# Performance work log

Hardware: AMD Instinct MI355X
Metric: run time of the kernel (lower is better)

The kernel has to match this reference:

```python
import jax, jax.numpy as jnp
import numpy as np

SEQ_LEN, BATCH, INPUT_DIM, HIDDEN_DIM = 2048, 16, 1024, 2048
COMPRESSION_RATIO = 0.5


def setup_inputs() -> dict:
    key = jax.random.key(0)
    ks = jax.random.split(key, 10)
    s_in = 0.02  # xavier-ish scale for (hidden, input) linears
    return {
        "x": jax.random.normal(ks[0], (SEQ_LEN, BATCH, INPUT_DIM), dtype=jnp.float32),
        "A": jax.random.normal(ks[1], (HIDDEN_DIM, HIDDEN_DIM), dtype=jnp.float32) * 0.1 - 0.5,
        "W_B": jax.random.normal(ks[2], (HIDDEN_DIM, INPUT_DIM), dtype=jnp.float32) * s_in,
        "W_C": jax.random.normal(ks[3], (HIDDEN_DIM, INPUT_DIM), dtype=jnp.float32) * s_in,
        "W_delta": jax.random.normal(ks[4], (HIDDEN_DIM, INPUT_DIM), dtype=jnp.float32) * s_in,
        "b_delta": jnp.zeros((HIDDEN_DIM,), dtype=jnp.float32),
        "W_in": jax.random.normal(ks[5], (HIDDEN_DIM, INPUT_DIM), dtype=jnp.float32) * s_in,
        "b_in": jnp.zeros((HIDDEN_DIM,), dtype=jnp.float32),
        "W_comp": jax.random.normal(ks[6], (INPUT_DIM, HIDDEN_DIM), dtype=jnp.float32) * s_in,
        "b_comp": jnp.zeros((INPUT_DIM,), dtype=jnp.float32),
    }


def reference(x, A, W_B, W_C, W_delta, b_delta, W_in, b_in, W_comp, b_comp):
    # x: (S, B, D_in).  A is an unused parameter in the original forward.
    seq_len = x.shape[0]
    compressed_len = max(1, int(seq_len * COMPRESSION_RATIO))
    step = seq_len // compressed_len

    # Batched projections over all timesteps (replaces per-step Linears)
    B_all = jnp.einsum('sbd,hd->sbh', x, W_B)                       # (S, B, H)
    C_all = jnp.einsum('sbd,hd->sbh', x, W_C)                       # (S, B, H)
    delta = jax.nn.softplus(jnp.einsum('sbd,hd->sbh', x, W_delta) + b_delta)
    u = jnp.einsum('sbd,hd->sbh', x, W_in) + b_in + B_all           # x_proj + B_t

    # Gated linear recurrence: h_t = (1 - delta_t) * h_{t-1} + delta_t * u_t
    def step_fn(h, inp):
        d, uu = inp
        h = (1.0 - d) * h + d * uu
        return h, h

    h0 = jnp.zeros((x.shape[1], u.shape[-1]), dtype=x.dtype)
    _, hs = jax.lax.scan(step_fn, h0, (delta, u))                   # (S, B, H)

    y = C_all * hs                                                  # (S, B, H)

    # Output at the last timestep of each window of size `step`
    idx = np.array([min(i + step, seq_len) - 1 for i in range(0, seq_len, step)])
    y_sel = y[idx]                                                  # (S_c, B, H)
    return jnp.einsum('sbh,dh->sbd', y_sel, W_comp) + b_comp        # (S_c, B, D_in)
```

## Files before the change

kernel.cpp:

```cpp
#include <hip/hip_runtime.h>
#include <hip/hip_bf16.h>
#include <cstdio>

#define S_LEN 2048
#define BATCH 16
#define D_INP 1024
#define H_DIM 2048
#define SC    (S_LEN / 2)
#define BH    (BATCH * H_DIM)
#define NC    16
#define CS    (S_LEN / NC)

typedef __bf16 b16;
typedef __bf16 b16x8 __attribute__((ext_vector_type(8)));
typedef __bf16 b16x4 __attribute__((ext_vector_type(4)));
typedef float  f32x4 __attribute__((ext_vector_type(4)));

__device__ __forceinline__ int sw_off(int r, int k8) {
  return r * 32 + ((k8 ^ ((r >> 1) & 3)) << 3);
}

__device__ __forceinline__ void gl2lds16(const b16* g, b16* l) {
  __builtin_amdgcn_global_load_lds(
      (const __attribute__((address_space(1))) void*)g,
      (__attribute__((address_space(3))) void*)l, 16, 0, 0);
}

__device__ __forceinline__ float softplus_fast(float t) {
  float e = __expf(-fabsf(t));
  return fmaxf(t, 0.f) + __logf(1.f + e);
}

__global__ void cvt_x_kernel(const float* __restrict__ in, b16* __restrict__ out, int n4) {
  int i = blockIdx.x * 256 + threadIdx.x;
  if (i >= n4) return;
  float4 v = ((const float4*)in)[i];
  b16x4 o = {(b16)v.x, (b16)v.y, (b16)v.z, (b16)v.w};
  ((b16x4*)out)[i] = o;
}

__global__ void prep_w_kernel(const float* __restrict__ Wd, const float* __restrict__ Win,
                              const float* __restrict__ WB, const float* __restrict__ Wc,
                              const float* __restrict__ Wcp,
                              b16* __restrict__ Wdu, b16* __restrict__ Wcb,
                              b16* __restrict__ Wcpb) {
  const int HD4 = (H_DIM * D_INP) / 4;
  int i = blockIdx.x * 256 + threadIdx.x;
  if (i >= HD4) return;
  float4 a = ((const float4*)Wd)[i];
  float4 b = ((const float4*)Win)[i];
  float4 c = ((const float4*)WB)[i];
  float4 d = ((const float4*)Wc)[i];
  float4 e = ((const float4*)Wcp)[i];
  ((b16x4*)Wdu)[i] = {(b16)a.x, (b16)a.y, (b16)a.z, (b16)a.w};
  ((b16x4*)Wdu)[HD4 + i] = {(b16)(b.x + c.x), (b16)(b.y + c.y), (b16)(b.z + c.z), (b16)(b.w + c.w)};
  ((b16x4*)Wcb)[i] = {(b16)d.x, (b16)d.y, (b16)d.z, (b16)d.w};
  ((b16x4*)Wcpb)[i] = {(b16)e.x, (b16)e.y, (b16)e.z, (b16)e.w};
}

#define AH0 0
#define AH1 8192
#define BH0 16384
#define BH1 24576

template <int MODE>
__device__ __forceinline__ void stage_half(const b16* __restrict__ G, int ldg,
                                           int base_row, int kcol, b16* half_base,
                                           int wave, int lane, bool isA) {
#pragma unroll
  for (int q = 0; q < 2; ++q) {
    const int rbase = q * 128 + wave * 16;
    const int r = rbase + (lane >> 2);
    const int p = lane & 3;
    const int gl = p ^ ((r >> 1) & 3);
    long grow = base_row + r;
    if (MODE == 1 && isA) grow = 2 * grow - (grow & 15) + 16;
    gl2lds16(G + grow * (long)ldg + kcol + gl * 8, half_base + rbase * 32);
  }
}

template <int MODE>
__global__ __launch_bounds__(512, 2) void gemm8p(
    const b16* __restrict__ A, const b16* __restrict__ W, int K,
    const float* __restrict__ bias0, const float* __restrict__ bias1,
    const b16* __restrict__ hsel, b16* __restrict__ ob0, b16* __restrict__ ob1,
    float* __restrict__ of) {
  extern __shared__ b16 lds[];
  const int tid  = threadIdx.x;
  const int lane = tid & 63;
  const int wave = tid >> 6;
  const int wm = wave >> 2, wn = wave & 3;
  const int lm = lane & 15;
  const int l8 = lane >> 4;

  const int gx  = gridDim.x;
  const int nwg = gx * gridDim.y;
  const int id0 = blockIdx.y * gx + blockIdx.x;
  const int sw  = (id0 & 7) * (nwg >> 3) + (id0 >> 3);
  const int m0 = (sw / gx) * 256;
  const int n0 = (sw % gx) * 256;

  f32x4 acc[8][4];
#pragma unroll
  for (int i = 0; i < 8; i++)
#pragma unroll
    for (int j = 0; j < 4; j++) acc[i][j] = (f32x4)0.f;

  const int NT = K >> 6;

  {
    b16* B0 = lds;
    stage_half<MODE>(A, K, m0, 0,  B0 + AH0, wave, lane, true);
    stage_half<MODE>(W, K, n0, 0,  B0 + BH0, wave, lane, false);
    stage_half<MODE>(A, K, m0, 32, B0 + AH1, wave, lane, true);
    stage_half<MODE>(W, K, n0, 32, B0 + BH1, wave, lane, false);
    asm volatile("s_waitcnt vmcnt(4)" ::: "memory");
    __builtin_amdgcn_s_barrier();
  }

  for (int t = 0; t < NT; ++t) {
    b16* const C = lds + ((t & 1) << 15);
    b16* const N = lds + (((t + 1) & 1) << 15);
    const int kn = (t + 1) << 6;
    const bool pf = (t + 1 < NT);
    b16x8 a[8], bb0, bb1;

#pragma unroll
    for (int i = 0; i < 8; i++)
      a[i] = *(const b16x8*)(C + AH0 + sw_off(wm * 128 + i * 16 + lm, l8));
    bb0 = *(const b16x8*)(C + BH0 + sw_off(wn * 64 + 0 + lm, l8));
    bb1 = *(const b16x8*)(C + BH0 + sw_off(wn * 64 + 16 + lm, l8));
    if (pf) stage_half<MODE>(A, K, m0, kn, N + AH0, wave, lane, true);
    __builtin_amdgcn_s_barrier();
    asm volatile("s_waitcnt lgkmcnt(0)" ::: "memory");
    __builtin_amdgcn_sched_barrier(0);
    __builtin_amdgcn_s_setprio(1);
#pragma unroll
    for (int i = 0; i < 8; i++) {
      acc[i][0] = __builtin_amdgcn_mfma_f32_16x16x32_bf16(a[i], bb0, acc[i][0], 0, 0, 0);
      acc[i][1] = __builtin_amdgcn_mfma_f32_16x16x32_bf16(a[i], bb1, acc[i][1], 0, 0, 0);
    }
    __builtin_amdgcn_s_setprio(0);
    __builtin_amdgcn_s_barrier();

    bb0 = *(const b16x8*)(C + BH0 + sw_off(wn * 64 + 32 + lm, l8));
    bb1 = *(const b16x8*)(C + BH0 + sw_off(wn * 64 + 48 + lm, l8));
    if (pf) {
      stage_half<MODE>(W, K, n0, kn, N + BH0, wave, lane, false);
      asm volatile("s_waitcnt vmcnt(4)" ::: "memory");
    } else {
      asm volatile("s_waitcnt vmcnt(0)" ::: "memory");
    }
    __builtin_amdgcn_s_barrier();
    asm volatile("s_waitcnt lgkmcnt(0)" ::: "memory");
    __builtin_amdgcn_sched_barrier(0);
    __builtin_amdgcn_s_setprio(1);
#pragma unroll
    for (int i = 0; i < 8; i++) {
      acc[i][2] = __builtin_amdgcn_mfma_f32_16x16x32_bf16(a[i], bb0, acc[i][2], 0, 0, 0);
      acc[i][3] = __builtin_amdgcn_mfma_f32_16x16x32_bf16(a[i], bb1, acc[i][3], 0, 0, 0);
    }
    __builtin_amdgcn_s_setprio(0);
    __builtin_amdgcn_s_barrier();

#pragma unroll
    for (int i = 0; i < 8; i++)
      a[i] = *(const b16x8*)(C + AH1 + sw_off(wm * 128 + i * 16 + lm, l8));
    bb0 = *(const b16x8*)(C + BH1 + sw_off(wn * 64 + 0 + lm, l8));
    bb1 = *(const b16x8*)(C + BH1 + sw_off(wn * 64 + 16 + lm, l8));
    if (pf) stage_half<MODE>(A, K, m0, kn + 32, N + AH1, wave, lane, true);
    __builtin_amdgcn_s_barrier();
    asm volatile("s_waitcnt lgkmcnt(0)" ::: "memory");
    __builtin_amdgcn_sched_barrier(0);
    __builtin_amdgcn_s_setprio(1);
#pragma unroll
    for (int i = 0; i < 8; i++) {
      acc[i][0] = __builtin_amdgcn_mfma_f32_16x16x32_bf16(a[i], bb0, acc[i][0], 0, 0, 0);
      acc[i][1] = __builtin_amdgcn_mfma_f32_16x16x32_bf16(a[i], bb1, acc[i][1], 0, 0, 0);
    }
    __builtin_amdgcn_s_setprio(0);
    __builtin_amdgcn_s_barrier();

    bb0 = *(const b16x8*)(C + BH1 + sw_off(wn * 64 + 32 + lm, l8));
    bb1 = *(const b16x8*)(C + BH1 + sw_off(wn * 64 + 48 + lm, l8));
    if (pf) {
      stage_half<MODE>(W, K, n0, kn + 32, N + BH1, wave, lane, false);
      asm volatile("s_waitcnt vmcnt(4)" ::: "memory");
    }
    __builtin_amdgcn_s_barrier();
    asm volatile("s_waitcnt lgkmcnt(0)" ::: "memory");
    __builtin_amdgcn_sched_barrier(0);
    __builtin_amdgcn_s_setprio(1);
#pragma unroll
    for (int i = 0; i < 8; i++) {
      acc[i][2] = __builtin_amdgcn_mfma_f32_16x16x32_bf16(a[i], bb0, acc[i][2], 0, 0, 0);
      acc[i][3] = __builtin_amdgcn_mfma_f32_16x16x32_bf16(a[i], bb1, acc[i][3], 0, 0, 0);
    }
    __builtin_amdgcn_s_setprio(0);
    __builtin_amdgcn_s_barrier();
  }

  if (MODE == 0) {
    const bool is_delta = (n0 < H_DIM);
    const float* bias = is_delta ? bias0 : bias1;
    b16* ob = is_delta ? ob0 : ob1;
    const int nc0 = (n0 & (H_DIM - 1)) + wn * 64 + lm;
    float bv[4];
#pragma unroll
    for (int j = 0; j < 4; j++) bv[j] = bias[nc0 + j * 16];
#pragma unroll
    for (int i = 0; i < 8; i++) {
      const long rb = m0 + wm * 128 + i * 16 + l8 * 4;
      b16* pr = ob + rb * H_DIM + nc0;
      if (is_delta) {
#pragma unroll
        for (int j = 0; j < 4; j++)
#pragma unroll
          for (int rg = 0; rg < 4; ++rg)
            pr[(long)rg * H_DIM + j * 16] = (b16)softplus_fast(acc[i][j][rg] + bv[j]);
      } else {
#pragma unroll
        for (int j = 0; j < 4; j++)
#pragma unroll
          for (int rg = 0; rg < 4; ++rg)
            pr[(long)rg * H_DIM + j * 16] = (b16)(acc[i][j][rg] + bv[j]);
      }
    }
  } else if (MODE == 1) {
    const int nc0 = n0 + wn * 64 + lm;
#pragma unroll
    for (int i = 0; i < 8; i++) {
      const long rb = m0 + wm * 128 + i * 16 + l8 * 4;
      const b16* hp = hsel + rb * H_DIM + nc0;
      b16* pr = ob0 + rb * H_DIM + nc0;
#pragma unroll
      for (int j = 0; j < 4; j++)
#pragma unroll
        for (int rg = 0; rg < 4; ++rg) {
          float hv = (float)hp[(long)rg * H_DIM + j * 16];
          pr[(long)rg * H_DIM + j * 16] = (b16)(acc[i][j][rg] * hv);
        }
    }
  } else {
    const int nc0 = n0 + wn * 64 + lm;
    float bv[4];
#pragma unroll
    for (int j = 0; j < 4; j++) bv[j] = bias0[nc0 + j * 16];
#pragma unroll
    for (int i = 0; i < 8; i++) {
      const long rb = m0 + wm * 128 + i * 16 + l8 * 4;
      float* pr = of + rb * D_INP + nc0;
#pragma unroll
      for (int j = 0; j < 4; j++)
#pragma unroll
        for (int rg = 0; rg < 4; ++rg)
          pr[(long)rg * D_INP + j * 16] = acc[i][j][rg] + bv[j];
    }
  }
}

__device__ __forceinline__ int sw_off128(int r, int k8) {
  return r * 32 + ((k8 ^ ((r >> 1) & 3)) << 3);
}

template <int MODE>
__global__ __launch_bounds__(256, 2) void gemm_bt(
    const b16* __restrict__ A, const b16* __restrict__ W, int K,
    const float* __restrict__ bias0, const float* __restrict__ bias1,
    const b16* __restrict__ hsel, b16* __restrict__ ob0, b16* __restrict__ ob1,
    float* __restrict__ of) {
  __shared__ b16 As[128 * 32];
  __shared__ b16 Bs[128 * 32];
  const int tid  = threadIdx.x;
  const int lane = tid & 63;
  const int wave = tid >> 6;
  const int wr = wave >> 1, wc = wave & 1;
  const int m0 = blockIdx.y * 128;
  const int n0 = blockIdx.x * 128;
  const int lm = lane & 15;
  const int l8 = lane >> 4;
  const int rL  = wave * 16 + (lane >> 2);
  const int k8p = lane & 3;

  f32x4 acc[4][4];
#pragma unroll
  for (int i = 0; i < 4; i++)
#pragma unroll
    for (int j = 0; j < 4; j++) acc[i][j] = (f32x4)0.f;

  for (int k0 = 0; k0 < K; k0 += 32) {
#pragma unroll
    for (int hh = 0; hh < 2; ++hh) {
      const int r = rL + hh * 64;
      const int k8l = k8p ^ ((r >> 1) & 3);
      b16* ldsA = As + (wave * 16 + hh * 64) * 32;
      b16* ldsB = Bs + (wave * 16 + hh * 64) * 32;
      long arow = m0 + r;
      if (MODE == 1) arow = 2 * arow - (arow & 15) + 16;
      gl2lds16(A + arow * (long)K + k0 + k8l * 8, ldsA);
      gl2lds16(W + (long)(n0 + r) * K + k0 + k8l * 8, ldsB);
    }
    __syncthreads();
    b16x8 af[4], bfr[4];
#pragma unroll
    for (int i = 0; i < 4; i++) af[i] = *(const b16x8*)(As + sw_off128(wr * 64 + i * 16 + lm, l8));
#pragma unroll
    for (int j = 0; j < 4; j++) bfr[j] = *(const b16x8*)(Bs + sw_off128(wc * 64 + j * 16 + lm, l8));
#pragma unroll
    for (int i = 0; i < 4; i++)
#pragma unroll
      for (int j = 0; j < 4; j++)
        acc[i][j] = __builtin_amdgcn_mfma_f32_16x16x32_bf16(af[i], bfr[j], acc[i][j], 0, 0, 0);
    __syncthreads();
  }

  if (MODE == 0) {
    const bool is_delta = (n0 < H_DIM);
    const float* bias = is_delta ? bias0 : bias1;
    b16* ob = is_delta ? ob0 : ob1;
    const int nc0 = (n0 & (H_DIM - 1)) + wc * 64 + lm;
    float bv[4];
#pragma unroll
    for (int j = 0; j < 4; j++) bv[j] = bias[nc0 + j * 16];
#pragma unroll
    for (int i = 0; i < 4; i++) {
      const long rb = m0 + wr * 64 + i * 16 + l8 * 4;
      b16* pr = ob + rb * H_DIM + nc0;
      if (is_delta) {
#pragma unroll
        for (int j = 0; j < 4; j++)
#pragma unroll
          for (int rg = 0; rg < 4; ++rg)
            pr[(long)rg * H_DIM + j * 16] = (b16)softplus_fast(acc[i][j][rg] + bv[j]);
      } else {
#pragma unroll
        for (int j = 0; j < 4; j++)
#pragma unroll
          for (int rg = 0; rg < 4; ++rg)
            pr[(long)rg * H_DIM + j * 16] = (b16)(acc[i][j][rg] + bv[j]);
      }
    }
  } else if (MODE == 1) {
    const int nc0 = n0 + wc * 64 + lm;
#pragma unroll
    for (int i = 0; i < 4; i++) {
      const long rb = m0 + wr * 64 + i * 16 + l8 * 4;
      const b16* hp = hsel + rb * H_DIM + nc0;
      b16* pr = ob0 + rb * H_DIM + nc0;
#pragma unroll
      for (int j = 0; j < 4; j++)
#pragma unroll
        for (int rg = 0; rg < 4; ++rg) {
          float hv = (float)hp[(long)rg * H_DIM + j * 16];
          pr[(long)rg * H_DIM + j * 16] = (b16)(acc[i][j][rg] * hv);
        }
    }
  } else {
    const int nc0 = n0 + wc * 64 + lm;
    float bv[4];
#pragma unroll
    for (int j = 0; j < 4; j++) bv[j] = bias0[nc0 + j * 16];
#pragma unroll
    for (int i = 0; i < 4; i++) {
      const long rb = m0 + wr * 64 + i * 16 + l8 * 4;
      float* pr = of + rb * D_INP + nc0;
#pragma unroll
      for (int j = 0; j < 4; j++)
#pragma unroll
        for (int rg = 0; rg < 4; ++rg)
          pr[(long)rg * D_INP + j * 16] = acc[i][j][rg] + bv[j];
    }
  }
}

__global__ void scan_a_kernel(const b16* __restrict__ dl, const b16* __restrict__ uu,
                              float* __restrict__ P, float* __restrict__ Q) {
  int g = blockIdx.x * 256 + threadIdx.x;
  int c = g >> 15;
  int p = g & (BH - 1);
  const b16* dp = dl + (size_t)c * CS * BH + p;
  const b16* up = uu + (size_t)c * CS * BH + p;
  float h = 0.f, pr = 1.f;
#pragma unroll 4
  for (int s = 0; s < CS; ++s) {
    float d = (float)dp[(size_t)s * BH];
    float u = (float)up[(size_t)s * BH];
    float a = 1.f - d;
    h = a * h + d * u;
    pr *= a;
  }
  P[g] = pr;
  Q[g] = h;
}

__global__ void scan_b_kernel(const float* __restrict__ P, const float* __restrict__ Q,
                              float* __restrict__ Hs) {
  int p = blockIdx.x * 256 + threadIdx.x;
  float h = 0.f;
#pragma unroll
  for (int c = 0; c < NC; ++c) {
    Hs[c * BH + p] = h;
    h = P[c * BH + p] * h + Q[c * BH + p];
  }
}

__global__ void scan_c_kernel(const b16* __restrict__ dl, const b16* __restrict__ uu,
                              const float* __restrict__ Hs, b16* __restrict__ hsel) {
  int g = blockIdx.x * 256 + threadIdx.x;
  int c = g >> 15;
  int p = g & (BH - 1);
  const b16* dp = dl + (size_t)c * CS * BH + p;
  const b16* up = uu + (size_t)c * CS * BH + p;
  b16* hp = hsel + (size_t)(c * (CS / 2)) * BH + p;
  float h = Hs[g];
#pragma unroll 4
  for (int s = 0; s < CS; ++s) {
    float d = (float)dp[(size_t)s * BH];
    float u = (float)up[(size_t)s * BH];
    h = (1.f - d) * h + d * u;
    if (s & 1) hp[(size_t)(s >> 1) * BH] = (b16)h;
  }
}

extern "C" void kernel_launch(void* const* d_in, const int* in_sizes, int n_in,
                              void* d_out, int out_size, void* d_ws, size_t ws_size,
                              hipStream_t stream) {
  const float* x   = (const float*)d_in[0];
  const float* WB  = (const float*)d_in[2];
  const float* Wc  = (const float*)d_in[3];
  const float* Wd  = (const float*)d_in[4];
  const float* bd  = (const float*)d_in[5];
  const float* Win = (const float*)d_in[6];
  const float* bi  = (const float*)d_in[7];
  const float* Wcp = (const float*)d_in[8];
  const float* bc  = (const float*)d_in[9];
  float* out = (float*)d_out;

  char* w = (char*)d_ws;
  size_t off = 0;
  auto alloc = [&](size_t bytes) {
    void* p = w + off;
    off += (bytes + 255) & ~(size_t)255;
    return p;
  };
  b16* xb   = (b16*)alloc((size_t)S_LEN * BATCH * D_INP * 2);
  b16* Wdu  = (b16*)alloc((size_t)2 * H_DIM * D_INP * 2);
  b16* Wcb  = (b16*)alloc((size_t)H_DIM * D_INP * 2);
  b16* Wcpb = (b16*)alloc((size_t)D_INP * H_DIM * 2);
  b16* dbuf = (b16*)alloc((size_t)S_LEN * BH * 2);
  b16* ubuf = (b16*)alloc((size_t)S_LEN * BH * 2);
  b16* hsel = (b16*)alloc((size_t)SC * BH * 2);
  b16* ysel = (b16*)alloc((size_t)SC * BH * 2);
  float* P  = (float*)alloc((size_t)NC * BH * 4);
  float* Q  = (float*)alloc((size_t)NC * BH * 4);
  float* Hs = (float*)alloc((size_t)NC * BH * 4);
  if (off > ws_size) {
    fprintf(stderr, "kernel_launch: ws too small: need %zu have %zu\n", off, ws_size);
    return;
  }

  static int g_big = -1;
  if (g_big < 0) {
    hipError_t e0 = hipFuncSetAttribute(reinterpret_cast<const void*>(&gemm8p<0>),
                                        hipFuncAttributeMaxDynamicSharedMemorySize, 131072);
    hipError_t e1 = hipFuncSetAttribute(reinterpret_cast<const void*>(&gemm8p<1>),
                                        hipFuncAttributeMaxDynamicSharedMemorySize, 131072);
    hipError_t e2 = hipFuncSetAttribute(reinterpret_cast<const void*>(&gemm8p<2>),
                                        hipFuncAttributeMaxDynamicSharedMemorySize, 131072);
    g_big = (e0 == hipSuccess && e1 == hipSuccess && e2 == hipSuccess) ? 1 : 0;
  }

  int n4 = S_LEN * BATCH * D_INP / 4;
  cvt_x_kernel<<<(n4 + 255) / 256, 256, 0, stream>>>(x, xb, n4);
  int hd4 = H_DIM * D_INP / 4;
  prep_w_kernel<<<(hd4 + 255) / 256, 256, 0, stream>>>(Wd, Win, WB, Wc, Wcp, Wdu, Wcb, Wcpb);
  if (g_big) {
    dim3 g1(2 * H_DIM / 256, S_LEN * BATCH / 256);
    gemm8p<0><<<g1, 512, 131072, stream>>>(xb, Wdu, D_INP, bd, bi, nullptr, dbuf, ubuf, nullptr);
  } else {
    dim3 g1(2 * H_DIM / 128, S_LEN * BATCH / 128);
    gemm_bt<0><<<g1, 256, 0, stream>>>(xb, Wdu, D_INP, bd, bi, nullptr, dbuf, ubuf, nullptr);
  }
  scan_a_kernel<<<NC * BH / 256, 256, 0, stream>>>(dbuf, ubuf, P, Q);
  scan_b_kernel<<<BH / 256, 256, 0, stream>>>(P, Q, Hs);
  scan_c_kernel<<<NC * BH / 256, 256, 0, stream>>>(dbuf, ubuf, Hs, hsel);
  if (g_big) {
    dim3 g2(H_DIM / 256, SC * BATCH / 256);
    gemm8p<1><<<g2, 512, 131072, stream>>>(xb, Wcb, D_INP, nullptr, nullptr, hsel, ysel, nullptr, nullptr);
  } else {
    dim3 g2(H_DIM / 128, SC * BATCH / 128);
    gemm_bt<1><<<g2, 256, 0, stream>>>(xb, Wcb, D_INP, nullptr, nullptr, hsel, ysel, nullptr, nullptr);
  }
  if (g_big) {
    dim3 g3(D_INP / 256, SC * BATCH / 256);
    gemm8p<2><<<g3, 512, 131072, stream>>>(ysel, Wcpb, H_DIM, bc, nullptr, nullptr, nullptr, nullptr, out);
  } else {
    dim3 g3(D_INP / 128, SC * BATCH / 128);
    gemm_bt<2><<<g3, 256, 0, stream>>>(ysel, Wcpb, H_DIM, bc, nullptr, nullptr, nullptr, nullptr, out);
  }
}
```

Measured before the change: 811.7 us.

## Reorder GEMM main loop into 4x4 MFMA quadrants and vectorize scan kernels

```diff
diff --git a/kernel.cpp b/kernel.cpp
--- a/kernel.cpp
+++ b/kernel.cpp
@@ -8,6 +8,7 @@
 #define H_DIM 2048
 #define SC    (S_LEN / 2)
 #define BH    (BATCH * H_DIM)
+#define BH8   (BH / 8)
 #define NC    16
 #define CS    (S_LEN / NC)
 
@@ -31,12 +32,14 @@
   return fmaxf(t, 0.f) + __logf(1.f + e);
 }
 
-__global__ void cvt_x_kernel(const float* __restrict__ in, b16* __restrict__ out, int n4) {
+__global__ void cvt_x_kernel(const float* __restrict__ in, b16* __restrict__ out, int n8) {
   int i = blockIdx.x * 256 + threadIdx.x;
-  if (i >= n4) return;
-  float4 v = ((const float4*)in)[i];
-  b16x4 o = {(b16)v.x, (b16)v.y, (b16)v.z, (b16)v.w};
-  ((b16x4*)out)[i] = o;
+  if (i >= n8) return;
+  float4 v0 = ((const float4*)in)[i * 2];
+  float4 v1 = ((const float4*)in)[i * 2 + 1];
+  b16x8 o = {(b16)v0.x, (b16)v0.y, (b16)v0.z, (b16)v0.w,
+             (b16)v1.x, (b16)v1.y, (b16)v1.z, (b16)v1.w};
+  ((b16x8*)out)[i] = o;
 }
 
 __global__ void prep_w_kernel(const float* __restrict__ Wd, const float* __restrict__ Win,
@@ -79,6 +82,18 @@
   }
 }
 
+#define MFMA16(AF, BF, ROW0)                                                       \
+  do {                                                                             \
+    __builtin_amdgcn_s_setprio(1);                                                 \
+    _Pragma("unroll") for (int i_ = 0; i_ < 4; i_++) {                             \
+      _Pragma("unroll") for (int j_ = 0; j_ < 4; j_++) {                           \
+        acc[ROW0 + i_][j_] = __builtin_amdgcn_mfma_f32_16x16x32_bf16(              \
+            AF[i_], BF[j_], acc[ROW0 + i_][j_], 0, 0, 0);                          \
+      }                                                                            \
+    }                                                                              \
+    __builtin_amdgcn_s_setprio(0);                                                 \
+  } while (0)
+
 template <int MODE>
 __global__ __launch_bounds__(512, 2) void gemm8p(
     const b16* __restrict__ A, const b16* __restrict__ W, int K,
@@ -108,14 +123,21 @@
 
   const int NT = K >> 6;
 
+  b16x8 aE[4], aO[4], b0f[4], b1f[4];
+
   {
-    b16* B0 = lds;
-    stage_half<MODE>(A, K, m0, 0,  B0 + AH0, wave, lane, true);
-    stage_half<MODE>(W, K, n0, 0,  B0 + BH0, wave, lane, false);
-    stage_half<MODE>(A, K, m0, 32, B0 + AH1, wave, lane, true);
-    stage_half<MODE>(W, K, n0, 32, B0 + BH1, wave, lane, false);
+    stage_half<MODE>(A, K, m0, 0,  lds + AH0, wave, lane, true);
+    stage_half<MODE>(W, K, n0, 0,  lds + BH0, wave, lane, false);
+    stage_half<MODE>(A, K, m0, 32, lds + AH1, wave, lane, true);
+    stage_half<MODE>(W, K, n0, 32, lds + BH1, wave, lane, false);
     asm volatile("s_waitcnt vmcnt(4)" ::: "memory");
     __builtin_amdgcn_s_barrier();
+#pragma unroll
+    for (int i = 0; i < 4; i++)
+      aE[i] = *(const b16x8*)(lds + AH0 + sw_off(wm * 128 + i * 16 + lm, l8));
+#pragma unroll
+    for (int j = 0; j < 4; j++)
+      b0f[j] = *(const b16x8*)(lds + BH0 + sw_off(wn * 64 + j * 16 + lm, l8));
   }
 
   for (int t = 0; t < NT; ++t) {
@@ -123,28 +145,17 @@
     b16* const N = lds + (((t + 1) & 1) << 15);
     const int kn = (t + 1) << 6;
     const bool pf = (t + 1 < NT);
-    b16x8 a[8], bb0, bb1;
-
-#pragma unroll
-    for (int i = 0; i < 8; i++)
-      a[i] = *(const b16x8*)(C + AH0 + sw_off(wm * 128 + i * 16 + lm, l8));
-    bb0 = *(const b16x8*)(C + BH0 + sw_off(wn * 64 + 0 + lm, l8));
-    bb1 = *(const b16x8*)(C + BH0 + sw_off(wn * 64 + 16 + lm, l8));
+
     if (pf) stage_half<MODE>(A, K, m0, kn, N + AH0, wave, lane, true);
     __builtin_amdgcn_s_barrier();
-    asm volatile("s_waitcnt lgkmcnt(0)" ::: "memory");
+#pragma unroll
+    for (int i = 0; i < 4; i++)
+      aO[i] = *(const b16x8*)(C + AH0 + sw_off(wm * 128 + 64 + i * 16 + lm, l8));
+    asm volatile("s_waitcnt lgkmcnt(4)" ::: "memory");
     __builtin_amdgcn_sched_barrier(0);
-    __builtin_amdgcn_s_setprio(1);
-#pragma unroll
-    for (int i = 0; i < 8; i++) {
-      acc[i][0] = __builtin_amdgcn_mfma_f32_16x16x32_bf16(a[i], bb0, acc[i][0], 0, 0, 0);
-      acc[i][1] = __builtin_amdgcn_mfma_f32_16x16x32_bf16(a[i], bb1, acc[i][1], 0, 0, 0);
-    }
-    __builtin_amdgcn_s_setprio(0);
-    __builtin_amdgcn_s_barrier();
-
-    bb0 = *(const b16x8*)(C + BH0 + sw_off(wn * 64 + 32 + lm, l8));
-    bb1 = *(const b16x8*)(C + BH0 + sw_off(wn * 64 + 48 + lm, l8));
+    MFMA16(aE, b0f, 0);
+    __builtin_amdgcn_s_barrier();
+
     if (pf) {
       stage_half<MODE>(W, K, n0, kn, N + BH0, wave, lane, false);
       asm volatile("s_waitcnt vmcnt(4)" ::: "memory");
@@ -152,51 +163,45 @@
       asm volatile("s_waitcnt vmcnt(0)" ::: "memory");
     }
     __builtin_amdgcn_s_barrier();
-    asm volatile("s_waitcnt lgkmcnt(0)" ::: "memory");
+#pragma unroll
+    for (int i = 0; i < 4; i++)
+      aE[i] = *(const b16x8*)(C + AH1 + sw_off(wm * 128 + i * 16 + lm, l8));
+#pragma unroll
+    for (int j = 0; j < 4; j++)
+      b1f[j] = *(const b16x8*)(C + BH1 + sw_off(wn * 64 + j * 16 + lm, l8));
+    asm volatile("s_waitcnt lgkmcnt(8)" ::: "memory");
     __builtin_amdgcn_sched_barrier(0);
-    __builtin_amdgcn_s_setprio(1);
-#pragma unroll
-    for (int i = 0; i < 8; i++) {
-      acc[i][2] = __builtin_amdgcn_mfma_f32_16x16x32_bf16(a[i], bb0, acc[i][2], 0, 0, 0);
-      acc[i][3] = __builtin_amdgcn_mfma_f32_16x16x32_bf16(a[i], bb1, acc[i][3], 0, 0, 0);
-    }
-    __builtin_amdgcn_s_setprio(0);
-    __builtin_amdgcn_s_barrier();
-
-#pragma unroll
-    for (int i = 0; i < 8; i++)
-      a[i] = *(const b16x8*)(C + AH1 + sw_off(wm * 128 + i * 16 + lm, l8));
-    bb0 = *(const b16x8*)(C + BH1 + sw_off(wn * 64 + 0 + lm, l8));
-    bb1 = *(const b16x8*)(C + BH1 + sw_off(wn * 64 + 16 + lm, l8));
+    MFMA16(aO, b0f, 4);
+    __builtin_amdgcn_s_barrier();
+
     if (pf) stage_half<MODE>(A, K, m0, kn + 32, N + AH1, wave, lane, true);
     __builtin_amdgcn_s_barrier();
-    asm volatile("s_waitcnt lgkmcnt(0)" ::: "memory");
+#pragma unroll
+    for (int i = 0; i < 4; i++)
+      aO[i] = *(const b16x8*)(C + AH1 + sw_off(wm * 128 + 64 + i * 16 + lm, l8));
+    asm volatile("s_waitcnt lgkmcnt(4)" ::: "memory");
     __builtin_amdgcn_sched_barrier(0);
-    __builtin_amdgcn_s_setprio(1);
-#pragma unroll
-    for (int i = 0; i < 8; i++) {
-      acc[i][0] = __builtin_amdgcn_mfma_f32_16x16x32_bf16(a[i], bb0, acc[i][0], 0, 0, 0);
-      acc[i][1] = __builtin_amdgcn_mfma_f32_16x16x32_bf16(a[i], bb1, acc[i][1], 0, 0, 0);
-    }
-    __builtin_amdgcn_s_setprio(0);
-    __builtin_amdgcn_s_barrier();
-
-    bb0 = *(const b16x8*)(C + BH1 + sw_off(wn * 64 + 32 + lm, l8));
-    bb1 = *(const b16x8*)(C + BH1 + sw_off(wn * 64 + 48 + lm, l8));
+    MFMA16(aE, b1f, 0);
+    __builtin_amdgcn_s_barrier();
+
     if (pf) {
       stage_half<MODE>(W, K, n0, kn + 32, N + BH1, wave, lane, false);
       asm volatile("s_waitcnt vmcnt(4)" ::: "memory");
     }
     __builtin_amdgcn_s_barrier();
-    asm volatile("s_waitcnt lgkmcnt(0)" ::: "memory");
+    if (pf) {
+#pragma unroll
+      for (int i = 0; i < 4; i++)
+        aE[i] = *(const b16x8*)(N + AH0 + sw_off(wm * 128 + i * 16 + lm, l8));
+#pragma unroll
+      for (int j = 0; j < 4; j++)
+        b0f[j] = *(const b16x8*)(N + BH0 + sw_off(wn * 64 + j * 16 + lm, l8));
+      asm volatile("s_waitcnt lgkmcnt(8)" ::: "memory");
+    } else {
+      asm volatile("s_waitcnt lgkmcnt(0)" ::: "memory");
+    }
     __builtin_amdgcn_sched_barrier(0);
-    __builtin_amdgcn_s_setprio(1);
-#pragma unroll
-    for (int i = 0; i < 8; i++) {
-      acc[i][2] = __builtin_amdgcn_mfma_f32_16x16x32_bf16(a[i], bb0, acc[i][2], 0, 0, 0);
-      acc[i][3] = __builtin_amdgcn_mfma_f32_16x16x32_bf16(a[i], bb1, acc[i][3], 0, 0, 0);
-    }
-    __builtin_amdgcn_s_setprio(0);
+    MFMA16(aO, b1f, 4);
     __builtin_amdgcn_s_barrier();
   }
 
@@ -257,10 +262,6 @@
           pr[(long)rg * D_INP + j * 16] = acc[i][j][rg] + bv[j];
     }
   }
-}
-
-__device__ __forceinline__ int sw_off128(int r, int k8) {
-  return r * 32 + ((k8 ^ ((r >> 1) & 3)) << 3);
 }
 
 template <int MODE>
@@ -303,9 +304,9 @@
     __syncthreads();
     b16x8 af[4], bfr[4];
 #pragma unroll
-    for (int i = 0; i < 4; i++) af[i] = *(const b16x8*)(As + sw_off128(wr * 64 + i * 16 + lm, l8));
-#pragma unroll
-    for (int j = 0; j < 4; j++) bfr[j] = *(const b16x8*)(Bs + sw_off128(wc * 64 + j * 16 + lm, l8));
+    for (int i = 0; i < 4; i++) af[i] = *(const b16x8*)(As + sw_off(wr * 64 + i * 16 + lm, l8));
+#pragma unroll
+    for (int j = 0; j < 4; j++) bfr[j] = *(const b16x8*)(Bs + sw_off(wc * 64 + j * 16 + lm, l8));
 #pragma unroll
     for (int i = 0; i < 4; i++)
 #pragma unroll
@@ -376,21 +377,29 @@
 __global__ void scan_a_kernel(const b16* __restrict__ dl, const b16* __restrict__ uu,
                               float* __restrict__ P, float* __restrict__ Q) {
   int g = blockIdx.x * 256 + threadIdx.x;
-  int c = g >> 15;
-  int p = g & (BH - 1);
-  const b16* dp = dl + (size_t)c * CS * BH + p;
-  const b16* up = uu + (size_t)c * CS * BH + p;
-  float h = 0.f, pr = 1.f;
-#pragma unroll 4
+  int c = g >> 12;
+  int p = g & (BH8 - 1);
+  const b16x8* dp = (const b16x8*)dl + (size_t)c * CS * BH8 + p;
+  const b16x8* up = (const b16x8*)uu + (size_t)c * CS * BH8 + p;
+  float h[8], pr[8];
+#pragma unroll
+  for (int e = 0; e < 8; ++e) { h[e] = 0.f; pr[e] = 1.f; }
+#pragma unroll 2
   for (int s = 0; s < CS; ++s) {
-    float d = (float)dp[(size_t)s * BH];
-    float u = (float)up[(size_t)s * BH];
-    float a = 1.f - d;
-    h = a * h + d * u;
-    pr *= a;
-  }
-  P[g] = pr;
-  Q[g] = h;
+    b16x8 dv = dp[(size_t)s * BH8];
+    b16x8 uv = up[(size_t)s * BH8];
+#pragma unroll
+    for (int e = 0; e < 8; ++e) {
+      float d = (float)dv[e], u = (float)uv[e];
+      float a = 1.f - d;
+      h[e] = a * h[e] + d * u;
+      pr[e] *= a;
+    }
+  }
+  ((f32x4*)P)[g * 2 + 0] = {pr[0], pr[1], pr[2], pr[3]};
+  ((f32x4*)P)[g * 2 + 1] = {pr[4], pr[5], pr[6], pr[7]};
+  ((f32x4*)Q)[g * 2 + 0] = {h[0], h[1], h[2], h[3]};
+  ((f32x4*)Q)[g * 2 + 1] = {h[4], h[5], h[6], h[7]};
 }
 
 __global__ void scan_b_kernel(const float* __restrict__ P, const float* __restrict__ Q,
@@ -407,18 +416,28 @@
 __global__ void scan_c_kernel(const b16* __restrict__ dl, const b16* __restrict__ uu,
                               const float* __restrict__ Hs, b16* __restrict__ hsel) {
   int g = blockIdx.x * 256 + threadIdx.x;
-  int c = g >> 15;
-  int p = g & (BH - 1);
-  const b16* dp = dl + (size_t)c * CS * BH + p;
-  const b16* up = uu + (size_t)c * CS * BH + p;
-  b16* hp = hsel + (size_t)(c * (CS / 2)) * BH + p;
-  float h = Hs[g];
-#pragma unroll 4
+  int c = g >> 12;
+  int p = g & (BH8 - 1);
+  const b16x8* dp = (const b16x8*)dl + (size_t)c * CS * BH8 + p;
+  const b16x8* up = (const b16x8*)uu + (size_t)c * CS * BH8 + p;
+  b16x8* hp = (b16x8*)hsel + (size_t)c * (CS / 2) * BH8 + p;
+  f32x4 h0a = ((const f32x4*)(Hs + (size_t)c * BH))[p * 2];
+  f32x4 h0b = ((const f32x4*)(Hs + (size_t)c * BH))[p * 2 + 1];
+  float h[8] = {h0a[0], h0a[1], h0a[2], h0a[3], h0b[0], h0b[1], h0b[2], h0b[3]};
+#pragma unroll 2
   for (int s = 0; s < CS; ++s) {
-    float d = (float)dp[(size_t)s * BH];
-    float u = (float)up[(size_t)s * BH];
-    h = (1.f - d) * h + d * u;
-    if (s & 1) hp[(size_t)(s >> 1) * BH] = (b16)h;
+    b16x8 dv = dp[(size_t)s * BH8];
+    b16x8 uv = up[(size_t)s * BH8];
+#pragma unroll
+    for (int e = 0; e < 8; ++e) {
+      float d = (float)dv[e], u = (float)uv[e];
+      h[e] = (1.f - d) * h[e] + d * u;
+    }
+    if (s & 1) {
+      b16x8 o = {(b16)h[0], (b16)h[1], (b16)h[2], (b16)h[3],
+                 (b16)h[4], (b16)h[5], (b16)h[6], (b16)h[7]};
+      hp[(size_t)(s >> 1) * BH8] = o;
+    }
   }
 }
 
@@ -470,8 +489,8 @@
     g_big = (e0 == hipSuccess && e1 == hipSuccess && e2 == hipSuccess) ? 1 : 0;
   }
 
-  int n4 = S_LEN * BATCH * D_INP / 4;
-  cvt_x_kernel<<<(n4 + 255) / 256, 256, 0, stream>>>(x, xb, n4);
+  int n8 = S_LEN * BATCH * D_INP / 8;
+  cvt_x_kernel<<<(n8 + 255) / 256, 256, 0, stream>>>(x, xb, n8);
   int hd4 = H_DIM * D_INP / 4;
   prep_w_kernel<<<(hd4 + 255) / 256, 256, 0, stream>>>(Wd, Win, WB, Wc, Wcp, Wdu, Wcb, Wcpb);
   if (g_big) {
@@ -481,9 +500,9 @@
     dim3 g1(2 * H_DIM / 128, S_LEN * BATCH / 128);
     gemm_bt<0><<<g1, 256, 0, stream>>>(xb, Wdu, D_INP, bd, bi, nullptr, dbuf, ubuf, nullptr);
   }
-  scan_a_kernel<<<NC * BH / 256, 256, 0, stream>>>(dbuf, ubuf, P, Q);
+  scan_a_kernel<<<NC * BH8 / 256, 256, 0, stream>>>(dbuf, ubuf, P, Q);
   scan_b_kernel<<<BH / 256, 256, 0, stream>>>(P, Q, Hs);
-  scan_c_kernel<<<NC * BH / 256, 256, 0, stream>>>(dbuf, ubuf, Hs, hsel);
+  scan_c_kernel<<<NC * BH8 / 256, 256, 0, stream>>>(dbuf, ubuf, Hs, hsel);
   if (g_big) {
     dim3 g2(H_DIM / 256, SC * BATCH / 256);
     gemm8p<1><<<g2, 512, 131072, stream>>>(xb, Wcb, D_INP, nullptr, nullptr, hsel, ysel, nullptr, nullptr);
```

Result: slower. 834.1 us (+2.8%).
